# Kernel optimization log

Measured on AMD Instinct MI355X. Metric: run time of the kernel, lower is better.

The kernel has to match this reference:

```python
import jax, jax.numpy as jnp
import numpy as np

PS = 14            # patch size
EMBED = 1024       # vision embed dim
LLM = 2048         # llm embed dim
DS = 2             # downsample factor
B = 8
GRID = 64          # H = W = 64 patches per image
MAX_POS = 4096
ROPE_THETA = 10000.0


def _rope_cache(dim, max_pos, base):
    inv_freq = 1.0 / (base ** (jnp.arange(0, dim, 2, dtype=jnp.float32) / dim))
    t = jnp.arange(max_pos, dtype=jnp.float32)
    freqs = jnp.outer(t, inv_freq)  # [max_pos, dim//2]
    return jnp.cos(freqs), jnp.sin(freqs)


def setup_inputs() -> dict:
    key = jax.random.key(0)
    ks = jax.random.split(key, 5)
    n_total = B * GRID * GRID
    pixel_values = jax.random.normal(ks[0], (n_total, 3, PS, PS), jnp.float32)
    patch_w = jax.random.normal(ks[1], (EMBED, 3, PS, PS), jnp.float32) * (1.0 / np.sqrt(3 * PS * PS))
    patch_b = jax.random.normal(ks[2], (EMBED,), jnp.float32) * 0.02
    dense_w = jax.random.normal(ks[3], (LLM, EMBED, DS, DS), jnp.float32) * (1.0 / np.sqrt(EMBED * DS * DS))
    dense_b = jax.random.normal(ks[4], (LLM,), jnp.float32) * 0.02
    rope_dim = EMBED // 2
    cos_x, sin_x = _rope_cache(rope_dim, MAX_POS, ROPE_THETA)
    cos_y, sin_y = _rope_cache(rope_dim, MAX_POS, ROPE_THETA)
    grid_hw = jnp.full((B, 2), GRID, dtype=jnp.int32)
    return {"pixel_values": pixel_values, "grid_hw": grid_hw,
            "patch_w": patch_w, "patch_b": patch_b,
            "dense_w": dense_w, "dense_b": dense_b,
            "cos_x": cos_x, "sin_x": sin_x, "cos_y": cos_y, "sin_y": sin_y}


def _apply_rotary_1d(x, cos_c, sin_c, pos):
    # x: [N, d], cos_c/sin_c: [max_pos, d//2], pos: [N] int
    c = cos_c[pos]  # gather: [N, d//2]
    s = sin_c[pos]
    x1 = x[:, 0::2]
    x2 = x[:, 1::2]
    o1 = x1 * c - x2 * s
    o2 = x1 * s + x2 * c
    return jnp.stack([o1, o2], axis=-1).reshape(x.shape)  # re-interleave


def _positions(grid_np):
    # grid metadata is static host-side data; build per-patch (x, y) coords
    xs, ys = [], []
    for h, w in grid_np:
        pid = np.arange(h * w)
        xs.append(pid % w)
        ys.append(pid // w)
    return jnp.asarray(np.concatenate(xs)), jnp.asarray(np.concatenate(ys))


def reference(pixel_values, grid_hw, patch_w, patch_b, dense_w, dense_b,
              cos_x, sin_x, cos_y, sin_y):
    grid_np = np.asarray(grid_hw)
    # patchify conv (kernel == stride == patch) is a per-patch linear proj
    pe = jnp.einsum('nchw,echw->ne', pixel_values, patch_w) + patch_b  # [N, E]
    pe = jax.nn.gelu(pe, approximate=False)
    abs_x, abs_y = _positions(grid_np)
    half = EMBED // 2
    p1 = _apply_rotary_1d(pe[:, :half], cos_x, sin_x, abs_x)
    p2 = _apply_rotary_1d(pe[:, half:], cos_y, sin_y, abs_y)
    pe = jnp.concatenate([p1, p2], axis=-1)  # [N, E]
    # per-image downsample conv (kernel == stride == DS): 2x2 block linear
    outs = []
    cur = 0
    for h, w in grid_np:
        x = pe[cur:cur + h * w].reshape(h // DS, DS, w // DS, DS, EMBED)
        o = jnp.einsum('hpwqe,oepq->hwo', x, dense_w) + dense_b
        outs.append(o.reshape(-1, LLM))
        cur += h * w
    return jnp.concatenate(outs, axis=0)
```

## Files before the change

### kernel.cpp

```cpp
#include <hip/hip_runtime.h>
#include <cstdint>


using f16x8 = __attribute__((ext_vector_type(8))) _Float16;
using f16x4 = __attribute__((ext_vector_type(4))) _Float16;
using f32x4 = __attribute__((ext_vector_type(4))) float;

__device__ __forceinline__ void gload_lds16(const void* g, void* l) {
  __builtin_amdgcn_global_load_lds(
      reinterpret_cast<const __attribute__((address_space(1))) unsigned int*>(
          reinterpret_cast<uintptr_t>(g)),
      reinterpret_cast<__attribute__((address_space(3))) unsigned int*>(
          reinterpret_cast<uintptr_t>(l)),
      16, 0, 0);
}

#define BAR   asm volatile("s_barrier" ::: "memory")
#define LGKM0 asm volatile("s_waitcnt lgkmcnt(0)" ::: "memory")
#define VM0   asm volatile("s_waitcnt vmcnt(0)" ::: "memory")

#define KP 640


__global__ void conv_w_kernel(const float* __restrict__ w1,
                              const float* __restrict__ w2,
                              _Float16* __restrict__ h1,
                              _Float16* __restrict__ h2) {
  const int bid = blockIdx.x;
  if (bid < 2560) {
    int i = bid * 256 + threadIdx.x;
    int e = i / KP;
    int k = i - e * KP;
    float v = (k < 588) ? w1[(size_t)e * 588 + k] : 0.0f;
    h1[i] = (_Float16)v;
  } else {
    int j = (bid - 2560) * 256 + threadIdx.x;
    int o = j >> 10;
    int e = j & 1023;
    const float4 v = *(const float4*)(w2 + (size_t)o * 4096 + e * 4);
    h2[(size_t)o * 4096 + e]        = (_Float16)v.x;
    h2[(size_t)o * 4096 + 1024 + e] = (_Float16)v.y;
    h2[(size_t)o * 4096 + 2048 + e] = (_Float16)v.z;
    h2[(size_t)o * 4096 + 3072 + e] = (_Float16)v.w;
  }
}


#define MFMA16(I0, J0, AV, BV)                                                \
  _Pragma("unroll") for (int i_ = 0; i_ < 4; ++i_)                            \
  _Pragma("unroll") for (int j_ = 0; j_ < 2; ++j_)                            \
  _Pragma("unroll") for (int k_ = 0; k_ < 2; ++k_)                            \
      acc[(I0) + i_][(J0) + j_] = __builtin_amdgcn_mfma_f32_16x16x32_f16(     \
          AV[i_][k_], BV[j_][k_], acc[(I0) + i_][(J0) + j_], 0, 0, 0);

#define TILE_BODY(sb)                                                         \
  {                                                                           \
    f16x8 a0[4][2], a1[4][2], vb0[2][2], vb1[2][2];                           \
    _Pragma("unroll") for (int i = 0; i < 4; ++i) {                           \
      a0[i][0] = *(const f16x8*)(lbase + (sb) + aoff + i * 2048 + so0);       \
      a0[i][1] = *(const f16x8*)(lbase + (sb) + aoff + i * 2048 + so1);       \
    }                                                                         \
    _Pragma("unroll") for (int j = 0; j < 2; ++j) {                           \
      vb0[j][0] = *(const f16x8*)(lbase + (sb) + boff + j * 2048 + so0);      \
      vb0[j][1] = *(const f16x8*)(lbase + (sb) + boff + j * 2048 + so1);      \
    }                                                                         \
    MFMA16(0, 0, a0, vb0);                                                    \
    _Pragma("unroll") for (int j = 0; j < 2; ++j) {                           \
      vb1[j][0] = *(const f16x8*)(lbase + (sb) + boff + (2+j) * 2048 + so0);  \
      vb1[j][1] = *(const f16x8*)(lbase + (sb) + boff + (2+j) * 2048 + so1);  \
    }                                                                         \
    MFMA16(0, 2, a0, vb1);                                                    \
    _Pragma("unroll") for (int i = 0; i < 4; ++i) {                           \
      a1[i][0] = *(const f16x8*)(lbase + (sb) + aoff + (4+i) * 2048 + so0);   \
      a1[i][1] = *(const f16x8*)(lbase + (sb) + aoff + (4+i) * 2048 + so1);   \
    }                                                                         \
    MFMA16(4, 2, a1, vb1);                                                    \
    MFMA16(4, 0, a1, vb0);                                                    \
  }


__global__ __launch_bounds__(512, 2) void patch_gemm20(
    const float* __restrict__ pix,
    const _Float16* __restrict__ b1w,
    const float* __restrict__ bias1,
    const float* __restrict__ cosx, const float* __restrict__ sinx,
    const float* __restrict__ cosy, const float* __restrict__ siny,
    _Float16* __restrict__ peM)
{
  __shared__ _Float16 lds[2][2][256][64];

  const int tid  = threadIdx.x;
  const int lane = tid & 63;
  const int wave = tid >> 6;
  const int wm = wave >> 2, wn = wave & 3;
  const int bm = blockIdx.x, bn = blockIdx.y;
  const int l15 = lane & 15;
  const int g   = lane >> 4;
  const int s7  = l15 & 7;

  const char* lbase = (const char*)lds;
  char*       lw    = (char*)lds;
  const unsigned aoff = (unsigned)(wm * 16384 + l15 * 128);
  const unsigned boff = (unsigned)(32768 + wn * 8192 + l15 * 128);
  const unsigned so0  = (unsigned)(((0 + g) ^ s7) * 16);
  const unsigned so1  = (unsigned)(((4 + g) ^ s7) * 16);

  const int bm256 = bm * 256, bn256 = bn * 256;
  const int srow = wave * 32 + (lane >> 3);
  const int acol = lane & 15;
  const int arw  = wave * 32 + (lane >> 4);

  auto LOADA = [&](int s, float4 (&ar)[8]) {
    const bool full = (s < 9);
#pragma unroll
    for (int u = 0; u < 8; ++u) {
      const int row = arw + u * 4;
      const float* p = pix + (size_t)(bm256 + row) * 588 + s * 64 + acol * 4;
      if (full || acol < 3) ar[u] = *(const float4*)p;
      else ar[u] = make_float4(0.f, 0.f, 0.f, 0.f);
    }
  };
  auto WRITEA = [&](int s, float4 (&ar)[8]) {
    char* slot = lw + ((size_t)((s) & 1) << 16);
    const int c   = acol >> 1;
    const int sub = acol & 1;
#pragma unroll
    for (int u = 0; u < 8; ++u) {
      const int row = arw + u * 4;
      f16x4 v;
      v[0] = (_Float16)ar[u].x; v[1] = (_Float16)ar[u].y;
      v[2] = (_Float16)ar[u].z; v[3] = (_Float16)ar[u].w;
      *(f16x4*)(slot + row * 128 + ((c ^ (row & 7)) * 16 + sub * 8)) = v;
    }
  };
  auto STAGE_B = [&](int s) {
    char* slot = lw + ((size_t)((s) & 1) << 16);
    const int c0 = s * 64;
#pragma unroll
    for (int u = 0; u < 4; ++u) {
      const int row  = srow + u * 8;
      const int gcol = (lane & 7) ^ (row & 7);
      gload_lds16(b1w + (size_t)(bn256 + row) * KP + c0 + gcol * 8,
                  slot + 32768 + (wave * 4 + u) * 1024);
    }
  };

  f32x4 acc[8][4] = {};
  float4 areg[8];

  LOADA(0, areg); STAGE_B(0);
  VM0; WRITEA(0, areg); LGKM0; BAR;

  for (int s = 0; s < 10; ++s) {
    const unsigned sb = (unsigned)((s & 1) << 16);
    const bool st = (s + 1 < 10);
    if (st) { LOADA(s + 1, areg); STAGE_B(s + 1); }
    __builtin_amdgcn_s_setprio(1);
    TILE_BODY(sb);
    __builtin_amdgcn_s_setprio(0);
    if (st) { VM0; WRITEA(s + 1, areg); }
    LGKM0; BAR;
  }

  BAR;
  float* sw = (float*)(lw) + wave * (32 * 65);
  const int md = (lane >> 4) * 4;
  const int rq = lane & 3;
  const int lr = lane >> 2;
#pragma unroll
  for (int p = 0; p < 4; ++p) {
#pragma unroll
    for (int i = 0; i < 2; ++i)
#pragma unroll
      for (int r = 0; r < 4; ++r) {
        const int lrow = i * 16 + md + r;
#pragma unroll
        for (int nf = 0; nf < 4; ++nf)
          sw[lrow * 65 + nf * 16 + l15] = acc[2 * p + i][nf][r];
      }
#pragma unroll
    for (int rr = 0; rr < 2; ++rr) {
      const int lrow = rr * 16 + lr;
      const int m   = bm256 + wm * 128 + p * 32 + lrow;
      const int pid = m & 4095;
      const int yy = pid >> 6, xx = pid & 63;
      const int t  = (m >> 12) * 1024 + (yy >> 1) * 32 + (xx >> 1);
      const int pq = (yy & 1) * 2 + (xx & 1);
      const int e0 = bn256 + wn * 64 + rq * 16;
      const int h2 = (e0 >= 512) ? 1 : 0;
      const int idx0 = (h2 ? (e0 - 512) : e0) >> 1;
      const int pos  = h2 ? yy : xx;
      const float* ct = (h2 ? cosy : cosx) + pos * 256 + idx0;
      const float* st = (h2 ? siny : sinx) + pos * 256 + idx0;
      const float4 c0 = *(const float4*)ct, c1 = *(const float4*)(ct + 4);
      const float4 s0 = *(const float4*)st, s1 = *(const float4*)(st + 4);
      const float4 b0 = *(const float4*)(bias1 + e0);
      const float4 b1 = *(const float4*)(bias1 + e0 + 4);
      const float4 b2 = *(const float4*)(bias1 + e0 + 8);
      const float4 b3 = *(const float4*)(bias1 + e0 + 12);
      const float bb[16] = {b0.x,b0.y,b0.z,b0.w, b1.x,b1.y,b1.z,b1.w,
                            b2.x,b2.y,b2.z,b2.w, b3.x,b3.y,b3.z,b3.w};
      float v[16];
#pragma unroll
      for (int j = 0; j < 16; ++j) {
        float x = sw[lrow * 65 + rq * 16 + j] + bb[j];
        v[j] = 0.5f * x * (1.0f + erff(x * 0.70710678118654752f));
      }
      const float cc[8] = {c0.x,c0.y,c0.z,c0.w, c1.x,c1.y,c1.z,c1.w};
      const float ss[8] = {s0.x,s0.y,s0.z,s0.w, s1.x,s1.y,s1.z,s1.w};
      _Float16 o[16];
#pragma unroll
      for (int k = 0; k < 8; ++k) {
        o[2*k]   = (_Float16)(v[2*k] * cc[k] - v[2*k+1] * ss[k]);
        o[2*k+1] = (_Float16)(v[2*k] * ss[k] + v[2*k+1] * cc[k]);
      }
      _Float16* dst = peM + (size_t)t * 4096 + pq * 1024 + e0;
      *(f16x8*)dst       = *(const f16x8*)&o[0];
      *(f16x8*)(dst + 8) = *(const f16x8*)&o[8];
    }
  }
}


__global__ __launch_bounds__(512, 2) void dense_gemm9(
    const _Float16* __restrict__ aM,
    const _Float16* __restrict__ bM,
    const float* __restrict__ bias2, float* __restrict__ out)
{
  __shared__ _Float16 lds[2][2][256][64];

  const int tid  = threadIdx.x;
  const int lane = tid & 63;
  const int wave = tid >> 6;
  const int wm = wave >> 2, wn = wave & 3;
  const int bm = blockIdx.x, bn = blockIdx.y;
  const int l15 = lane & 15;
  const int g   = lane >> 4;
  const int s7  = l15 & 7;

  const char* lbase = (const char*)lds;
  char*       lw    = (char*)lds;
  const unsigned aoff = (unsigned)(wm * 16384 + l15 * 128);
  const unsigned boff = (unsigned)(32768 + wn * 8192 + l15 * 128);
  const unsigned so0  = (unsigned)(((0 + g) ^ s7) * 16);
  const unsigned so1  = (unsigned)(((4 + g) ^ s7) * 16);

  const int bm256 = bm * 256, bn256 = bn * 256;
  const int srow = (wave * 4) * 8 + (lane >> 3);

  auto STAGE = [&](int s) {
    char* slot = lw + ((size_t)(s & 1) << 16);
    const int c0 = s * 64;
#pragma unroll
    for (int u = 0; u < 4; ++u) {
      const int row  = srow + u * 8;
      const int gcol = (lane & 7) ^ (row & 7);
      gload_lds16(aM + (size_t)(bm256 + row) * 4096 + c0 + gcol * 8,
                  slot + (wave * 4 + u) * 1024);
      gload_lds16(bM + (size_t)(bn256 + row) * 4096 + c0 + gcol * 8,
                  slot + 32768 + (wave * 4 + u) * 1024);
    }
  };

  f32x4 acc[8][4] = {};

  STAGE(0); VM0; BAR;
#pragma unroll 2
  for (int s = 0; s < 64; ++s) {
    if (s + 1 < 64) STAGE(s + 1);
    const unsigned sb = (unsigned)((s & 1) << 16);
    __builtin_amdgcn_s_setprio(1);
    TILE_BODY(sb);
    __builtin_amdgcn_s_setprio(0);
    LGKM0; VM0; BAR;
  }

  const int md = (lane >> 4) * 4;
  const int r0 = bm256 + wm * 128;
  const int c0 = bn256 + wn * 64;
#pragma unroll
  for (int nf = 0; nf < 4; ++nf) {
    const int o = c0 + nf * 16 + l15;
    const float bs = bias2[o];
#pragma unroll
    for (int mf = 0; mf < 8; ++mf) {
      const int t_ = r0 + mf * 16 + md;
#pragma unroll
      for (int r = 0; r < 4; ++r)
        out[(size_t)(t_ + r) * 2048 + o] = acc[mf][nf][r] + bs;
    }
  }
}


extern "C" void kernel_launch(void* const* d_in, const int* in_sizes, int n_in,
                              void* d_out, int out_size, void* d_ws, size_t ws_size,
                              hipStream_t stream) {
  const float* pix  = (const float*)d_in[0];
  const float* w1   = (const float*)d_in[2];
  const float* b1   = (const float*)d_in[3];
  const float* w2   = (const float*)d_in[4];
  const float* b2   = (const float*)d_in[5];
  const float* cosx = (const float*)d_in[6];
  const float* sinx = (const float*)d_in[7];
  const float* cosy = (const float*)d_in[8];
  const float* siny = (const float*)d_in[9];
  float* out = (float*)d_out;

  _Float16* ws = (_Float16*)d_ws;
  const size_t PE_N  = (size_t)8192 * 4096;
  const size_t B1_N  = (size_t)1024 * KP;
  _Float16* peM  = ws;
  _Float16* b1h  = peM + PE_N;
  _Float16* b2h  = b1h + B1_N;

  conv_w_kernel<<<dim3(2560 + 8192), dim3(256), 0, stream>>>(w1, w2, b1h, b2h);
  patch_gemm20<<<dim3(128, 4), dim3(512), 0, stream>>>(
      pix, b1h, b1, cosx, sinx, cosy, siny, peM);
  dense_gemm9<<<dim3(32, 8), dim3(512), 0, stream>>>(
      peM, b2h, b2, out);
}
```

Measured before the change: 245.8 us.

## Retile patch GEMM to 128x256 blocks with 256 threads and K=32 stages

Restructures the patch-projection GEMM from 256x256 tiles with 512 threads and 64-wide K steps to 128x256 tiles with 256 threads (2x2 waves) and 32-wide K steps over 19 stages. LDS use drops to 48KB with a new XOR swizzle. The epilogue now handles 32 columns per lane. The goal is more blocks per CU and finer K padding (608 vs 640) to cut wasted MFMA work, at the cost of more barriers per K and less B reuse per block.

New measurement: 254.1 us. +3.4%, slower.

```diff
diff --git a/kernel.cpp b/kernel.cpp
--- a/kernel.cpp
+++ b/kernel.cpp
@@ -79,7 +79,7 @@
   }
 
 
-__global__ __launch_bounds__(512, 2) void patch_gemm20(
+__global__ __launch_bounds__(256, 2) void patch_gemm21(
     const float* __restrict__ pix,
     const _Float16* __restrict__ b1w,
     const float* __restrict__ bias1,
@@ -87,136 +87,141 @@
     const float* __restrict__ cosy, const float* __restrict__ siny,
     _Float16* __restrict__ peM)
 {
-  __shared__ _Float16 lds[2][2][256][64];
+  __shared__ char lds[49152];
 
   const int tid  = threadIdx.x;
   const int lane = tid & 63;
   const int wave = tid >> 6;
-  const int wm = wave >> 2, wn = wave & 3;
+  const int wm = wave >> 1, wn = wave & 1;
   const int bm = blockIdx.x, bn = blockIdx.y;
   const int l15 = lane & 15;
   const int g   = lane >> 4;
-  const int s7  = l15 & 7;
-
-  const char* lbase = (const char*)lds;
-  char*       lw    = (char*)lds;
-  const unsigned aoff = (unsigned)(wm * 16384 + l15 * 128);
-  const unsigned boff = (unsigned)(32768 + wn * 8192 + l15 * 128);
-  const unsigned so0  = (unsigned)(((0 + g) ^ s7) * 16);
-  const unsigned so1  = (unsigned)(((4 + g) ^ s7) * 16);
-
-  const int bm256 = bm * 256, bn256 = bn * 256;
-  const int srow = wave * 32 + (lane >> 3);
-  const int acol = lane & 15;
-  const int arw  = wave * 32 + (lane >> 4);
-
-  auto LOADA = [&](int s, float4 (&ar)[8]) {
-    const bool full = (s < 9);
-#pragma unroll
-    for (int u = 0; u < 8; ++u) {
-      const int row = arw + u * 4;
-      const float* p = pix + (size_t)(bm256 + row) * 588 + s * 64 + acol * 4;
-      if (full || acol < 3) ar[u] = *(const float4*)p;
-      else ar[u] = make_float4(0.f, 0.f, 0.f, 0.f);
+
+  const int bm128 = bm * 128, bn256 = bn * 256;
+
+  const unsigned xr  = (unsigned)((l15 & 3) ^ ((l15 >> 2) & 3));
+  const unsigned soX = ((unsigned)g ^ xr) * 16u;
+  const unsigned aoff = (unsigned)(wm * 4096 + l15 * 64);
+  const unsigned boff = (unsigned)(8192 + wn * 8192 + l15 * 64);
+
+  const int arow = tid >> 1, ah = tid & 1;
+  const int axr  = (arow & 3) ^ ((arow >> 2) & 3);
+  const int bgc  = (lane & 3) ^ ((lane >> 2) & 3) ^ ((lane >> 4) & 3);
+
+  auto LOADA = [&](int s, float4 (&ar)[4]) {
+    const bool full = (s < 18);
+#pragma unroll
+    for (int q = 0; q < 4; ++q) {
+      const int col = s * 32 + ah * 16 + q * 4;
+      if (full || col + 4 <= 588)
+        ar[q] = *(const float4*)(pix + (size_t)(bm128 + arow) * 588 + col);
+      else
+        ar[q] = make_float4(0.f, 0.f, 0.f, 0.f);
     }
   };
-  auto WRITEA = [&](int s, float4 (&ar)[8]) {
-    char* slot = lw + ((size_t)((s) & 1) << 16);
-    const int c   = acol >> 1;
-    const int sub = acol & 1;
-#pragma unroll
-    for (int u = 0; u < 8; ++u) {
-      const int row = arw + u * 4;
-      f16x4 v;
-      v[0] = (_Float16)ar[u].x; v[1] = (_Float16)ar[u].y;
-      v[2] = (_Float16)ar[u].z; v[3] = (_Float16)ar[u].w;
-      *(f16x4*)(slot + row * 128 + ((c ^ (row & 7)) * 16 + sub * 8)) = v;
+  auto WRITEA = [&](int s, float4 (&ar)[4]) {
+    char* slot = lds + (s & 1) * 24576;
+#pragma unroll
+    for (int cp = 0; cp < 2; ++cp) {
+      f16x8 v;
+      v[0] = (_Float16)ar[2*cp].x; v[1] = (_Float16)ar[2*cp].y;
+      v[2] = (_Float16)ar[2*cp].z; v[3] = (_Float16)ar[2*cp].w;
+      v[4] = (_Float16)ar[2*cp+1].x; v[5] = (_Float16)ar[2*cp+1].y;
+      v[6] = (_Float16)ar[2*cp+1].z; v[7] = (_Float16)ar[2*cp+1].w;
+      const int c = 2 * ah + cp;
+      *(f16x8*)(slot + arow * 64 + ((c ^ axr) * 16)) = v;
     }
   };
   auto STAGE_B = [&](int s) {
-    char* slot = lw + ((size_t)((s) & 1) << 16);
-    const int c0 = s * 64;
+    char* slot = lds + (s & 1) * 24576;
 #pragma unroll
     for (int u = 0; u < 4; ++u) {
-      const int row  = srow + u * 8;
-      const int gcol = (lane & 7) ^ (row & 7);
-      gload_lds16(b1w + (size_t)(bn256 + row) * KP + c0 + gcol * 8,
-                  slot + 32768 + (wave * 4 + u) * 1024);
+      const int b16 = wave * 4 + u;
+      const int row = b16 * 16 + (lane >> 2);
+      gload_lds16(b1w + (size_t)(bn256 + row) * KP + s * 32 + bgc * 8,
+                  slot + 8192 + b16 * 1024);
     }
   };
 
-  f32x4 acc[8][4] = {};
-  float4 areg[8];
+  f32x4 acc[4][8] = {};
+  float4 areg[4];
 
   LOADA(0, areg); STAGE_B(0);
   VM0; WRITEA(0, areg); LGKM0; BAR;
 
-  for (int s = 0; s < 10; ++s) {
-    const unsigned sb = (unsigned)((s & 1) << 16);
-    const bool st = (s + 1 < 10);
+  for (int s = 0; s < 19; ++s) {
+    const int sb = (s & 1) * 24576;
+    const bool st = (s + 1 < 19);
     if (st) { LOADA(s + 1, areg); STAGE_B(s + 1); }
     __builtin_amdgcn_s_setprio(1);
-    TILE_BODY(sb);
+    f16x8 a[4], b[8];
+#pragma unroll
+    for (int i = 0; i < 4; ++i)
+      a[i] = *(const f16x8*)(lds + sb + aoff + i * 1024 + soX);
+#pragma unroll
+    for (int j = 0; j < 8; ++j)
+      b[j] = *(const f16x8*)(lds + sb + boff + j * 1024 + soX);
+#pragma unroll
+    for (int i = 0; i < 4; ++i)
+#pragma unroll
+      for (int j = 0; j < 8; ++j)
+        acc[i][j] = __builtin_amdgcn_mfma_f32_16x16x32_f16(
+            a[i], b[j], acc[i][j], 0, 0, 0);
     __builtin_amdgcn_s_setprio(0);
     if (st) { VM0; WRITEA(s + 1, areg); }
     LGKM0; BAR;
   }
 
-  BAR;
-  float* sw = (float*)(lw) + wave * (32 * 65);
+  float* sw = (float*)(lds) + wave * (16 * 129);
   const int md = (lane >> 4) * 4;
   const int rq = lane & 3;
   const int lr = lane >> 2;
 #pragma unroll
   for (int p = 0; p < 4; ++p) {
 #pragma unroll
-    for (int i = 0; i < 2; ++i)
-#pragma unroll
-      for (int r = 0; r < 4; ++r) {
-        const int lrow = i * 16 + md + r;
-#pragma unroll
-        for (int nf = 0; nf < 4; ++nf)
-          sw[lrow * 65 + nf * 16 + l15] = acc[2 * p + i][nf][r];
-      }
-#pragma unroll
-    for (int rr = 0; rr < 2; ++rr) {
-      const int lrow = rr * 16 + lr;
-      const int m   = bm256 + wm * 128 + p * 32 + lrow;
+    for (int r = 0; r < 4; ++r) {
+      const int lrow = md + r;
+#pragma unroll
+      for (int nf = 0; nf < 8; ++nf)
+        sw[lrow * 129 + nf * 16 + l15] = acc[p][nf][r];
+    }
+    {
+      const int m   = bm128 + wm * 64 + p * 16 + lr;
       const int pid = m & 4095;
       const int yy = pid >> 6, xx = pid & 63;
       const int t  = (m >> 12) * 1024 + (yy >> 1) * 32 + (xx >> 1);
       const int pq = (yy & 1) * 2 + (xx & 1);
-      const int e0 = bn256 + wn * 64 + rq * 16;
+      const int e0 = bn256 + wn * 128 + rq * 32;
       const int h2 = (e0 >= 512) ? 1 : 0;
       const int idx0 = (h2 ? (e0 - 512) : e0) >> 1;
       const int pos  = h2 ? yy : xx;
       const float* ct = (h2 ? cosy : cosx) + pos * 256 + idx0;
       const float* st = (h2 ? siny : sinx) + pos * 256 + idx0;
-      const float4 c0 = *(const float4*)ct, c1 = *(const float4*)(ct + 4);
-      const float4 s0 = *(const float4*)st, s1 = *(const float4*)(st + 4);
-      const float4 b0 = *(const float4*)(bias1 + e0);
-      const float4 b1 = *(const float4*)(bias1 + e0 + 4);
-      const float4 b2 = *(const float4*)(bias1 + e0 + 8);
-      const float4 b3 = *(const float4*)(bias1 + e0 + 12);
-      const float bb[16] = {b0.x,b0.y,b0.z,b0.w, b1.x,b1.y,b1.z,b1.w,
-                            b2.x,b2.y,b2.z,b2.w, b3.x,b3.y,b3.z,b3.w};
-      float v[16];
-#pragma unroll
-      for (int j = 0; j < 16; ++j) {
-        float x = sw[lrow * 65 + rq * 16 + j] + bb[j];
+      float cc[16], ss[16], bb[32];
+#pragma unroll
+      for (int q = 0; q < 4; ++q) {
+        *(float4*)&cc[q * 4] = *(const float4*)(ct + q * 4);
+        *(float4*)&ss[q * 4] = *(const float4*)(st + q * 4);
+      }
+#pragma unroll
+      for (int q = 0; q < 8; ++q)
+        *(float4*)&bb[q * 4] = *(const float4*)(bias1 + e0 + q * 4);
+      float v[32];
+#pragma unroll
+      for (int j = 0; j < 32; ++j) {
+        float x = sw[lr * 129 + rq * 32 + j] + bb[j];
         v[j] = 0.5f * x * (1.0f + erff(x * 0.70710678118654752f));
       }
-      const float cc[8] = {c0.x,c0.y,c0.z,c0.w, c1.x,c1.y,c1.z,c1.w};
-      const float ss[8] = {s0.x,s0.y,s0.z,s0.w, s1.x,s1.y,s1.z,s1.w};
-      _Float16 o[16];
-#pragma unroll
-      for (int k = 0; k < 8; ++k) {
+      _Float16 o[32];
+#pragma unroll
+      for (int k = 0; k < 16; ++k) {
         o[2*k]   = (_Float16)(v[2*k] * cc[k] - v[2*k+1] * ss[k]);
         o[2*k+1] = (_Float16)(v[2*k] * ss[k] + v[2*k+1] * cc[k]);
       }
       _Float16* dst = peM + (size_t)t * 4096 + pq * 1024 + e0;
-      *(f16x8*)dst       = *(const f16x8*)&o[0];
-      *(f16x8*)(dst + 8) = *(const f16x8*)&o[8];
+#pragma unroll
+      for (int q = 0; q < 4; ++q)
+        *(f16x8*)(dst + q * 8) = *(const f16x8*)&o[q * 8];
     }
   }
 }
@@ -315,7 +320,7 @@
   _Float16* b2h  = b1h + B1_N;
 
   conv_w_kernel<<<dim3(2560 + 8192), dim3(256), 0, stream>>>(w1, w2, b1h, b2h);
-  patch_gemm20<<<dim3(128, 4), dim3(512), 0, stream>>>(
+  patch_gemm21<<<dim3(256, 4), dim3(256), 0, stream>>>(
       pix, b1h, b1, cosx, sinx, cosy, siny, peM);
   dense_gemm9<<<dim3(32, 8), dim3(512), 0, stream>>>(
       peM, b2h, b2, out);
```
